# Optimization experiments

Hardware: AMD Instinct MI355X
Metric: run time of the kernel (lower is better)

## Reference

```python
import jax, jax.numpy as jnp
import numpy as np

NH, NL, NPNT = 8, 4, 4          # heads, levels, points
NQ, BS, NK, D, DFFN = 100, 8, 18, 256, 1024
SPATIAL = np.array([[92, 92], [46, 46], [23, 23], [12, 12]], np.int32)
LEN_MEM = int((SPATIAL[:, 0] * SPATIAL[:, 1]).sum())  # 11253


def _layernorm(x, g, b):
    m = x.mean(-1, keepdims=True)
    v = ((x - m) ** 2).mean(-1, keepdims=True)
    return (x - m) / jnp.sqrt(v + 1e-5) * g + b


def _mha(xq, xk, xv, in_w, in_b, out_w, out_b):
    # torch nn.MultiheadAttention semantics, inputs (S, B, D)
    S, B, d = xq.shape
    dh = d // NH
    wq, wk, wv = jnp.split(in_w, 3, axis=0)
    bq, bk, bv = jnp.split(in_b, 3, axis=0)
    def proj(x, w, b):
        return (x @ w.T + b).reshape(x.shape[0], B, NH, dh).transpose(1, 2, 0, 3)
    q = proj(xq, wq, bq) * (1.0 / np.sqrt(dh))
    k = proj(xk, wk, bk)
    v = proj(xv, wv, bv)
    att = jax.nn.softmax(jnp.einsum('bhqd,bhkd->bhqk', q, k), axis=-1)
    o = jnp.einsum('bhqk,bhkd->bhqd', att, v).transpose(2, 0, 1, 3).reshape(S, B, d)
    return o @ out_w.T + out_b


def _bilinear(v_l, loc):
    # v_l: (bs,H,W,NH,dh); loc: (bs,Lq,NH,P,2) normalized [0,1]
    # matches F.grid_sample(align_corners=False, padding_mode='zeros')
    bs, H, W, nh, dh = v_l.shape
    x = loc[..., 0] * W - 0.5
    y = loc[..., 1] * H - 0.5
    x0 = jnp.floor(x); y0 = jnp.floor(y)
    lx = x - x0; ly = y - y0
    b_idx = jnp.arange(bs)[:, None, None, None]
    h_idx = jnp.arange(nh)[None, None, :, None]
    def corner(xa, ya, w):
        valid = (xa >= 0) & (xa < W) & (ya >= 0) & (ya < H)
        xi = jnp.clip(xa, 0, W - 1).astype(jnp.int32)
        yi = jnp.clip(ya, 0, H - 1).astype(jnp.int32)
        return v_l[b_idx, yi, xi, h_idx] * (w * valid)[..., None]
    return (corner(x0, y0, (1 - lx) * (1 - ly)) + corner(x0 + 1, y0, lx * (1 - ly))
            + corner(x0, y0 + 1, (1 - lx) * ly) + corner(x0 + 1, y0 + 1, lx * ly))


def _msda(q, rp, mem, pad_mask, ss, off_w, off_b, aw_w, aw_b, val_w, val_b, outp_w, outp_b):
    bs, Lq, d = q.shape
    dh = d // NH
    value = mem @ val_w.T + val_b
    value = jnp.where(pad_mask[..., None], 0.0, value).reshape(bs, -1, NH, dh)
    off = (q @ off_w.T + off_b).reshape(bs, Lq, NH, NL, NPNT, 2)
    aw = jax.nn.softmax((q @ aw_w.T + aw_b).reshape(bs, Lq, NH, NL * NPNT), -1)
    aw = aw.reshape(bs, Lq, NH, NL, NPNT)
    wh = jnp.asarray(ss[:, ::-1].copy(), jnp.float32)  # offset normalizer (W, H)
    loc = rp[:, :, None, :, None, :] + off / wh[None, None, None, :, None, :]
    out = jnp.zeros((bs, Lq, NH, dh), q.dtype)
    start = 0
    for l in range(NL):
        H, W = int(ss[l, 0]), int(ss[l, 1])
        v_l = value[:, start:start + H * W].reshape(bs, H, W, NH, dh)
        start += H * W
        samp = _bilinear(v_l, loc[:, :, :, l])          # (bs,Lq,NH,P,dh)
        out = out + (samp * aw[:, :, :, l, :, None]).sum(3)
    return out.reshape(bs, Lq, d) @ outp_w.T + outp_b


def _forward(tgt_pose, pos, ref_points, memory, w_in_w, w_in_b, w_out_w, w_out_b,
             a_in_w, a_in_b, a_out_w, a_out_b, off_w, off_b, aw_w, aw_b,
             val_w, val_b, outp_w, outp_b, wn_g, wn_b, an_g, an_b,
             n1_g, n1_b, n2_g, n2_b, l1_w, l1_b, l2_w, l2_b,
             spatial_shapes, level_start_index, padding_mask):
    ss = np.asarray(jax.device_get(spatial_shapes))
    nq, bs, nk, d = tgt_pose.shape
    # within-group self-attn over the nk keypoint tokens.
    # NOTE: with_pos_embed mutates tgt_pose in place in the torch code, so
    # q = k = v = tgt + pos and the residual also uses tgt + pos (faithful).
    t = tgt_pose + pos
    x = t.reshape(nq * bs, nk, d).transpose(1, 0, 2)   # (nk, nq*bs, d)
    a1 = _mha(x, x, x, w_in_w, w_in_b, w_out_w, w_out_b)
    t = _layernorm(t + a1.transpose(1, 0, 2).reshape(nq, bs, nk, d), wn_g, wn_b)
    # across-group self-attn over the nq groups
    x2 = t.reshape(nq, bs * nk, d)
    a2 = _mha(x2, x2, x2, a_in_w, a_in_b, a_out_w, a_out_b)
    t = _layernorm(t + a2.reshape(nq, bs, nk, d), an_g, an_b)
    # MSDeformAttn cross-attention (in-place pos add again, faithful)
    t = t + pos
    q = t.transpose(1, 0, 2, 3).reshape(bs, nq * nk, d)
    rp = jnp.swapaxes(ref_points, 0, 1)                # (bs, nq*nk, NL, 2)
    mem = jnp.swapaxes(memory, 0, 1)                   # (bs, LEN_MEM, d)
    c = _msda(q, rp, mem, padding_mask, ss, off_w, off_b, aw_w, aw_b,
              val_w, val_b, outp_w, outp_b)
    c = c.reshape(bs, nq, nk, d).transpose(1, 0, 2, 3)
    t = _layernorm(t + c, n1_g, n1_b)
    # FFN (dropout is identity in eval)
    h = jax.nn.relu(t @ l1_w.T + l1_b)
    return _layernorm(t + (h @ l2_w.T + l2_b), n2_g, n2_b)


def setup_inputs() -> dict:
    key = jax.random.key(0)
    ks = jax.random.split(key, 16)
    p = lambda k, shape: jax.random.normal(k, shape, jnp.float32) * 0.02
    lsi = np.concatenate([[0], np.cumsum(SPATIAL[:, 0] * SPATIAL[:, 1])[:-1]]).astype(np.int32)
    return {
        'tgt_pose': jax.random.normal(ks[0], (NQ, BS, NK, D), jnp.float32),
        'pos': jax.random.normal(ks[1], (NQ, BS, NK, D), jnp.float32),
        'ref_points': jax.random.uniform(ks[2], (NQ * NK, BS, NL, 2), jnp.float32),
        'memory': jax.random.normal(ks[3], (LEN_MEM, BS, D), jnp.float32),
        'w_in_w': p(ks[4], (3 * D, D)), 'w_in_b': jnp.zeros((3 * D,)),
        'w_out_w': p(ks[5], (D, D)), 'w_out_b': jnp.zeros((D,)),
        'a_in_w': p(ks[6], (3 * D, D)), 'a_in_b': jnp.zeros((3 * D,)),
        'a_out_w': p(ks[7], (D, D)), 'a_out_b': jnp.zeros((D,)),
        'off_w': p(ks[8], (NH * NL * NPNT * 2, D)),
        'off_b': jax.random.uniform(ks[9], (NH * NL * NPNT * 2,), jnp.float32, -2.0, 2.0),
        'aw_w': p(ks[10], (NH * NL * NPNT, D)), 'aw_b': jnp.zeros((NH * NL * NPNT,)),
        'val_w': p(ks[11], (D, D)), 'val_b': jnp.zeros((D,)),
        'outp_w': p(ks[12], (D, D)), 'outp_b': jnp.zeros((D,)),
        'wn_g': jnp.ones((D,)), 'wn_b': jnp.zeros((D,)),
        'an_g': jnp.ones((D,)), 'an_b': jnp.zeros((D,)),
        'n1_g': jnp.ones((D,)), 'n1_b': jnp.zeros((D,)),
        'n2_g': jnp.ones((D,)), 'n2_b': jnp.zeros((D,)),
        'l1_w': p(ks[13], (DFFN, D)), 'l1_b': jnp.zeros((DFFN,)),
        'l2_w': p(ks[14], (D, DFFN)), 'l2_b': jnp.zeros((D,)),
        'spatial_shapes': jnp.asarray(SPATIAL),
        'level_start_index': jnp.asarray(lsi),
        'padding_mask': jnp.zeros((BS, LEN_MEM), bool),
    }


def reference(tgt_pose, pos, ref_points, memory, w_in_w, w_in_b, w_out_w, w_out_b,
              a_in_w, a_in_b, a_out_w, a_out_b, off_w, off_b, aw_w, aw_b,
              val_w, val_b, outp_w, outp_b, wn_g, wn_b, an_g, an_b,
              n1_g, n1_b, n2_g, n2_b, l1_w, l1_b, l2_w, l2_b,
              spatial_shapes, level_start_index, padding_mask):
    return _forward(tgt_pose, pos, ref_points, memory, w_in_w, w_in_b, w_out_w, w_out_b,
                    a_in_w, a_in_b, a_out_w, a_out_b, off_w, off_b, aw_w, aw_b,
                    val_w, val_b, outp_w, outp_b, wn_g, wn_b, an_g, an_b,
                    n1_g, n1_b, n2_g, n2_b, l1_w, l1_b, l2_w, l2_b,
                    spatial_shapes, level_start_index, padding_mask)
```

## Files before the change

kernel.cpp:

```cpp
#include <hip/hip_runtime.h>
#include <math.h>

#define NH_ 8
#define D_ 256
#define NK_ 18
#define NQ_ 100
#define BS_ 8
#define LQ_ 1800
#define LEN_MEM_ 11253
#define NTOK_ 14400

typedef short bf16x8 __attribute__((ext_vector_type(8)));
typedef float f32x4 __attribute__((ext_vector_type(4)));
typedef unsigned short ushort;

__device__ inline ushort f2bf(float f) {
    unsigned int u = __builtin_bit_cast(unsigned int, f);
    unsigned int r = (u + 0x7fffu + ((u >> 16) & 1u)) >> 16;
    return (ushort)r;
}
__device__ inline float bf2f(unsigned int u16) {
    unsigned int i = u16 << 16;
    return __builtin_bit_cast(float, i);
}

__global__ __launch_bounds__(256)
void wcvt_kernel(const float* s0, const float* s1, const float* s2, const float* s3,
                 const float* s4, const float* s5, const float* s6, const float* s7,
                 const float* s8, const float* s9, ushort* dst) {
    const int sizes[10] = {196608,65536,196608,65536,65536,32768,65536,65536,262144,262144};
    const int offs[10]  = {0,196608,262144,458752,524288,589824,622592,688128,753664,1015808};
    int ti = blockIdx.y;
    const float* s;
    switch (ti) {
        case 0: s = s0; break; case 1: s = s1; break; case 2: s = s2; break;
        case 3: s = s3; break; case 4: s = s4; break; case 5: s = s5; break;
        case 6: s = s6; break; case 7: s = s7; break; case 8: s = s8; break;
        default: s = s9; break;
    }
    int n = sizes[ti];
    int i = (blockIdx.x * 256 + threadIdx.x) * 8;
    if (i >= n) return;
    ushort* d = dst + offs[ti] + i;
    float4 f0 = *(const float4*)(s + i);
    float4 f1 = *(const float4*)(s + i + 4);
    int4 val;
    val.x = (int)f2bf(f0.x) | ((int)f2bf(f0.y) << 16);
    val.y = (int)f2bf(f0.z) | ((int)f2bf(f0.w) << 16);
    val.z = (int)f2bf(f1.x) | ((int)f2bf(f1.y) << 16);
    val.w = (int)f2bf(f1.z) | ((int)f2bf(f1.w) << 16);
    *(int4*)d = val;
}

__global__ __launch_bounds__(256)
void addcvt_kernel(const float* __restrict__ a, const float* __restrict__ b,
                   float* __restrict__ c, ushort* __restrict__ cbf, int n4) {
    int i = blockIdx.x * blockDim.x + threadIdx.x;
    if (i >= n4) return;
    float4 av = ((const float4*)a)[i];
    float4 bv = ((const float4*)b)[i];
    float4 cv;
    cv.x = av.x + bv.x; cv.y = av.y + bv.y; cv.z = av.z + bv.z; cv.w = av.w + bv.w;
    ((float4*)c)[i] = cv;
    uint2 p;
    p.x = (unsigned int)f2bf(cv.x) | ((unsigned int)f2bf(cv.y) << 16);
    p.y = (unsigned int)f2bf(cv.z) | ((unsigned int)f2bf(cv.w) << 16);
    *(uint2*)(cbf + (size_t)i * 4) = p;
}

template<int MODE, bool RELU, bool A_F32, bool OUT_BF16>
__global__ __launch_bounds__(256)
void gemm_kernel(const void* __restrict__ Av, const ushort* __restrict__ W,
                 const float* __restrict__ bias, void* __restrict__ Cv,
                 int M, int N, int K, const unsigned char* __restrict__ mask) {
    __shared__ ushort As[128 * 40];
    __shared__ ushort Bs[128 * 40];
    const int m0 = blockIdx.x * 128, n0 = blockIdx.y * 128;
    const int tid = threadIdx.x;
    const int w = tid >> 6, lane = tid & 63;
    const int wr = w >> 1, wc = w & 1;
    const int fr = lane & 15, hi = lane >> 4;
    f32x4 acc[4][4];
#pragma unroll
    for (int i = 0; i < 4; ++i)
#pragma unroll
        for (int j = 0; j < 4; ++j) acc[i][j] = f32x4{0.f, 0.f, 0.f, 0.f};

    for (int k0 = 0; k0 < K; k0 += 32) {
#pragma unroll
        for (int cc = 0; cc < 2; ++cc) {
            int c = tid + cc * 256;
            int row = c >> 2, kq = c & 3;
            int gr = m0 + row;
            int4 val = make_int4(0, 0, 0, 0);
            if (gr < M) {
                long arow;
                if (MODE == 1) {
                    int b = gr / LEN_MEM_; int m = gr - b * LEN_MEM_;
                    arow = (long)m * BS_ + b;
                } else if (MODE == 2) {
                    int b = gr / LQ_; int lq = gr - b * LQ_;
                    int q = lq / NK_; int kk = lq - q * NK_;
                    arow = (long)q * (BS_ * NK_) + b * NK_ + kk;
                } else {
                    arow = gr;
                }
                if (A_F32) {
                    const float* ap = (const float*)Av + arow * (long)K + k0 + kq * 8;
                    float4 f0 = *(const float4*)ap;
                    float4 f1 = *(const float4*)(ap + 4);
                    val.x = (int)f2bf(f0.x) | ((int)f2bf(f0.y) << 16);
                    val.y = (int)f2bf(f0.z) | ((int)f2bf(f0.w) << 16);
                    val.z = (int)f2bf(f1.x) | ((int)f2bf(f1.y) << 16);
                    val.w = (int)f2bf(f1.z) | ((int)f2bf(f1.w) << 16);
                } else {
                    val = *(const int4*)((const ushort*)Av + arow * (long)K + k0 + kq * 8);
                }
            }
            *(int4*)(As + row * 40 + kq * 8) = val;
        }
#pragma unroll
        for (int cc = 0; cc < 2; ++cc) {
            int c = tid + cc * 256;
            int row = c >> 2, kq = c & 3;
            *(int4*)(Bs + row * 40 + kq * 8) =
                *(const int4*)(W + (long)(n0 + row) * K + k0 + kq * 8);
        }
        __syncthreads();
        bf16x8 af[4], bfr[4];
#pragma unroll
        for (int i = 0; i < 4; ++i)
            af[i] = *(const bf16x8*)(As + (wr * 64 + i * 16 + fr) * 40 + hi * 8);
#pragma unroll
        for (int j = 0; j < 4; ++j)
            bfr[j] = *(const bf16x8*)(Bs + (wc * 64 + j * 16 + fr) * 40 + hi * 8);
#pragma unroll
        for (int i = 0; i < 4; ++i)
#pragma unroll
            for (int j = 0; j < 4; ++j)
                acc[i][j] = __builtin_amdgcn_mfma_f32_16x16x32_bf16(af[i], bfr[j], acc[i][j], 0, 0, 0);
        __syncthreads();
    }

#pragma unroll
    for (int i = 0; i < 4; ++i) {
#pragma unroll
        for (int r = 0; r < 4; ++r) {
            int gm = m0 + wr * 64 + i * 16 + hi * 4 + r;
            if (gm >= M) continue;
            long orow = gm;
            bool zero = false;
            if (MODE == 1) {
                if (mask && mask[gm]) zero = true;
            } else if (MODE == 3) {
                int b = gm / LQ_; int lq = gm - b * LQ_;
                int q = lq / NK_; int kk = lq - q * NK_;
                orow = (long)q * (BS_ * NK_) + b * NK_ + kk;
            }
#pragma unroll
            for (int j = 0; j < 4; ++j) {
                int gn = n0 + wc * 64 + j * 16 + fr;
                float v = acc[i][j][r] + bias[gn];
                if (RELU) v = fmaxf(v, 0.f);
                if (zero) v = 0.f;
                if (OUT_BF16) ((ushort*)Cv)[orow * (long)N + gn] = f2bf(v);
                else ((float*)Cv)[orow * (long)N + gn] = v;
            }
        }
    }
}

template<int S, int SP, int HPB>
__global__ __launch_bounds__(256)
void mattn_kernel(const ushort* __restrict__ qkv, ushort* __restrict__ outb,
                  int rsG, int rsS) {
    constexpr int SPk = ((SP + 31) / 32) * 32;
    constexpr int KST = 40;
    constexpr int PST = SPk + 8;
    constexpr int NT = SP / 16;
    constexpr int NB = HPB * NT;
    constexpr int HB = 8 / HPB;
    __shared__ ushort KsA[HPB * SP * KST];
    __shared__ ushort VtA[HPB * 32 * PST];
    __shared__ ushort PA [HPB * SP * PST];

    const int tid = threadIdx.x;
    const int g = blockIdx.x / HB;
    const int hbase = (blockIdx.x % HB) * HPB;

    for (int idx = tid; idx < HPB * S * 4; idx += 256) {
        int hh = idx / (S * 4); int rem = idx - hh * (S * 4);
        int j = rem >> 2, q = rem & 3;
        const ushort* base = qkv + ((size_t)g * rsG + (size_t)j * rsS) * 768 + (hbase + hh) * 32 + q * 8;
        uint4 kv = *(const uint4*)(base + 256);
        ushort* kd = KsA + hh * (SP * KST) + j * KST + q * 8;
        *(uint2*)kd = make_uint2(kv.x, kv.y);
        *(uint2*)(kd + 4) = make_uint2(kv.z, kv.w);
        uint4 vv = *(const uint4*)(base + 512);
        ushort* vt = VtA + hh * (32 * PST) + j;
        unsigned int uu[4] = {vv.x, vv.y, vv.z, vv.w};
#pragma unroll
        for (int e = 0; e < 4; ++e) {
            vt[(q * 8 + e * 2    ) * PST] = (ushort)(uu[e] & 0xffff);
            vt[(q * 8 + e * 2 + 1) * PST] = (ushort)(uu[e] >> 16);
        }
    }
    for (int idx = tid; idx < HPB * 32 * (SPk - S); idx += 256) {
        int hh = idx / (32 * (SPk - S)); int rem = idx - hh * (32 * (SPk - S));
        int d = rem / (SPk - S); int c = S + rem - d * (SPk - S);
        VtA[hh * 32 * PST + d * PST + c] = 0;
    }
    if constexpr (SPk > SP) {
        constexpr int PW = SPk - SP;
        for (int idx = tid; idx < HPB * SP * PW; idx += 256) {
            int hh = idx / (SP * PW); int rem = idx - hh * (SP * PW);
            int rrow = rem / PW; int c = SP + rem - rrow * PW;
            PA[hh * SP * PST + rrow * PST + c] = 0;
        }
    }
    __syncthreads();

    const int wv = tid >> 6, lane = tid & 63, fr = lane & 15, hi = lane >> 4;
    for (int band = wv; band < NB; band += 4) {
        const int hh = band / NT, mb = band - (band / NT) * NT;
        const int h = hbase + hh;
        const ushort* Ks = KsA + hh * (SP * KST);
        const ushort* Vt = VtA + hh * (32 * PST);
        ushort* P = PA + hh * (SP * PST);

        int sq = mb * 16 + fr; if (sq > S - 1) sq = S - 1;
        bf16x8 qf = *(const bf16x8*)(qkv + ((size_t)g * rsG + (size_t)sq * rsS) * 768 + h * 32 + hi * 8);
        f32x4 sc[NT];
#pragma unroll
        for (int t = 0; t < NT; ++t) {
            bf16x8 kf = *(const bf16x8*)(Ks + (t * 16 + fr) * KST + hi * 8);
            sc[t] = __builtin_amdgcn_mfma_f32_16x16x32_bf16(qf, kf, f32x4{0.f, 0.f, 0.f, 0.f}, 0, 0, 0);
        }
#pragma unroll
        for (int t = 0; t < NT; ++t) {
            bool valid = (t * 16 + fr) < S;
#pragma unroll
            for (int r = 0; r < 4; ++r)
                sc[t][r] = valid ? sc[t][r] * 0.17677669529663687f : -1e30f;
        }
#pragma unroll
        for (int r = 0; r < 4; ++r) {
            float m = sc[0][r];
#pragma unroll
            for (int t = 1; t < NT; ++t) m = fmaxf(m, sc[t][r]);
            m = fmaxf(m, __shfl_xor(m, 1)); m = fmaxf(m, __shfl_xor(m, 2));
            m = fmaxf(m, __shfl_xor(m, 4)); m = fmaxf(m, __shfl_xor(m, 8));
            float e[NT]; float sum = 0.f;
#pragma unroll
            for (int t = 0; t < NT; ++t) { e[t] = __expf(sc[t][r] - m); sum += e[t]; }
            sum += __shfl_xor(sum, 1); sum += __shfl_xor(sum, 2);
            sum += __shfl_xor(sum, 4); sum += __shfl_xor(sum, 8);
            float inv = 1.f / sum;
            int row = mb * 16 + hi * 4 + r;
#pragma unroll
            for (int t = 0; t < NT; ++t)
                P[row * PST + t * 16 + fr] = f2bf(e[t] * inv);
        }
        f32x4 o0 = {0.f, 0.f, 0.f, 0.f}, o1 = {0.f, 0.f, 0.f, 0.f};
#pragma unroll
        for (int kb = 0; kb < SPk / 32; ++kb) {
            bf16x8 pf = *(const bf16x8*)(P + (mb * 16 + fr) * PST + kb * 32 + hi * 8);
            bf16x8 v0 = *(const bf16x8*)(Vt + fr * PST + kb * 32 + hi * 8);
            bf16x8 v1 = *(const bf16x8*)(Vt + (16 + fr) * PST + kb * 32 + hi * 8);
            o0 = __builtin_amdgcn_mfma_f32_16x16x32_bf16(pf, v0, o0, 0, 0, 0);
            o1 = __builtin_amdgcn_mfma_f32_16x16x32_bf16(pf, v1, o1, 0, 0, 0);
        }
#pragma unroll
        for (int r = 0; r < 4; ++r) {
            int s = mb * 16 + hi * 4 + r;
            if (s < S) {
                size_t ob = ((size_t)g * rsG + (size_t)s * rsS) * 256 + h * 32;
                outb[ob + fr] = f2bf(o0[r]);
                outb[ob + 16 + fr] = f2bf(o1[r]);
            }
        }
    }
}

__global__ __launch_bounds__(256)
void addln_kernel(const float* __restrict__ base, const float* __restrict__ delta,
                  const float* __restrict__ gamma, const float* __restrict__ beta,
                  float* __restrict__ out, ushort* __restrict__ obf, int M) {
    int row = blockIdx.x * 4 + (threadIdx.x >> 6);
    int lane = threadIdx.x & 63;
    if (row >= M) return;
    const float* pb = base + (size_t)row * 256;
    const float* pd = delta + (size_t)row * 256;
    float v[4]; float s = 0.f;
#pragma unroll
    for (int i = 0; i < 4; ++i) { int c = lane + i * 64; v[i] = pb[c] + pd[c]; s += v[i]; }
#pragma unroll
    for (int off = 32; off; off >>= 1) s += __shfl_xor(s, off);
    float mean = s * (1.f / 256.f);
    float var = 0.f;
#pragma unroll
    for (int i = 0; i < 4; ++i) { float d = v[i] - mean; var += d * d; }
#pragma unroll
    for (int off = 32; off; off >>= 1) var += __shfl_xor(var, off);
    var *= (1.f / 256.f);
    float rstd = rsqrtf(var + 1e-5f);
#pragma unroll
    for (int i = 0; i < 4; ++i) {
        int c = lane + i * 64;
        float o = (v[i] - mean) * rstd * gamma[c] + beta[c];
        out[(size_t)row * 256 + c] = o;
        if (obf) obf[(size_t)row * 256 + c] = f2bf(o);
    }
}

__global__ __launch_bounds__(256)
void awsm_kernel(const float* __restrict__ aw, float* __restrict__ awn) {
    int u = blockIdx.x * 256 + threadIdx.x;
    if (u >= NTOK_ * 8) return;
    int row = u >> 3, h = u & 7;
    const float* p = aw + (size_t)row * 128 + h * 16;
    float w[16], m = -1e30f;
#pragma unroll
    for (int i = 0; i < 16; ++i) { w[i] = p[i]; m = fmaxf(m, w[i]); }
    float sum = 0.f;
#pragma unroll
    for (int i = 0; i < 16; ++i) { w[i] = __expf(w[i] - m); sum += w[i]; }
    float inv = 1.f / sum;
    float* o = awn + (size_t)u * 16;
#pragma unroll
    for (int i = 0; i < 16; ++i) o[i] = w[i] * inv;
}

__global__ __launch_bounds__(256)
void msda_kernel(const float* __restrict__ offb, const float* __restrict__ awn,
                 const ushort* __restrict__ val, const float* __restrict__ refp,
                 const int* __restrict__ spatial, const int* __restrict__ lsi,
                 ushort* __restrict__ samp) {
    int unit = blockIdx.x * 16 + (threadIdx.x >> 4);
    int lane = threadIdx.x & 15;
    int h = unit & 7;
    int t = unit >> 3;
    int lq = t % LQ_;
    int b = t / LQ_;
    const float* offp = offb + ((size_t)b * LQ_ + lq) * 256 + h * 32;
    const float* wp = awn + (size_t)unit * 16;
    float acc0 = 0.f, acc1 = 0.f;
#pragma unroll
    for (int lvl = 0; lvl < 4; ++lvl) {
        int H = spatial[lvl * 2], W = spatial[lvl * 2 + 1];
        int st = lsi[lvl];
        float rpx = refp[(((size_t)lq * BS_ + b) * 4 + lvl) * 2 + 0];
        float rpy = refp[(((size_t)lq * BS_ + b) * 4 + lvl) * 2 + 1];
        const ushort* vb = val + ((size_t)b * LEN_MEM_ + st) * 256 + h * 32 + lane * 2;
        float fW = (float)W, fH = (float)H;
#pragma unroll
        for (int p = 0; p < 4; ++p) {
            float ox = offp[(lvl * 4 + p) * 2 + 0];
            float oy = offp[(lvl * 4 + p) * 2 + 1];
            float x = rpx * fW + ox - 0.5f;
            float y = rpy * fH + oy - 0.5f;
            float x0f = floorf(x), y0f = floorf(y);
            float lx = x - x0f, ly = y - y0f;
            int x0 = (int)x0f, y0 = (int)y0f;
            int xc0 = min(max(x0, 0), W - 1), xc1 = min(max(x0 + 1, 0), W - 1);
            int yc0 = min(max(y0, 0), H - 1), yc1 = min(max(y0 + 1, 0), H - 1);
            float vx0 = (x0 >= 0 && x0 < W) ? 1.f : 0.f;
            float vx1 = (x0 >= -1 && x0 + 1 < W) ? 1.f : 0.f;
            float vy0 = (y0 >= 0 && y0 < H) ? 1.f : 0.f;
            float vy1 = (y0 >= -1 && y0 + 1 < H) ? 1.f : 0.f;
            float wpt = wp[lvl * 4 + p];
            float w00 = wpt * (1.f - lx) * (1.f - ly) * vx0 * vy0;
            float w10 = wpt * lx * (1.f - ly) * vx1 * vy0;
            float w01 = wpt * (1.f - lx) * ly * vx0 * vy1;
            float w11 = wpt * lx * ly * vx1 * vy1;
            unsigned int u00 = *(const unsigned int*)(vb + ((size_t)yc0 * W + xc0) * 256);
            unsigned int u10 = *(const unsigned int*)(vb + ((size_t)yc0 * W + xc1) * 256);
            unsigned int u01 = *(const unsigned int*)(vb + ((size_t)yc1 * W + xc0) * 256);
            unsigned int u11 = *(const unsigned int*)(vb + ((size_t)yc1 * W + xc1) * 256);
            acc0 += w00 * bf2f(u00 & 0xffff) + w10 * bf2f(u10 & 0xffff)
                  + w01 * bf2f(u01 & 0xffff) + w11 * bf2f(u11 & 0xffff);
            acc1 += w00 * bf2f(u00 >> 16) + w10 * bf2f(u10 >> 16)
                  + w01 * bf2f(u01 >> 16) + w11 * bf2f(u11 >> 16);
        }
    }
    size_t o = ((size_t)b * LQ_ + lq) * 256 + h * 32 + lane * 2;
    unsigned int pack = (unsigned int)f2bf(acc0) | ((unsigned int)f2bf(acc1) << 16);
    *(unsigned int*)(samp + o) = pack;
}

extern "C" void kernel_launch(void* const* d_in, const int* in_sizes, int n_in,
                              void* d_out, int out_size, void* d_ws, size_t ws_size,
                              hipStream_t stream) {
    const float* tgt     = (const float*)d_in[0];
    const float* pos     = (const float*)d_in[1];
    const float* refp    = (const float*)d_in[2];
    const float* memory  = (const float*)d_in[3];
    const float* w_in_w  = (const float*)d_in[4];
    const float* w_in_b  = (const float*)d_in[5];
    const float* w_out_w = (const float*)d_in[6];
    const float* w_out_b = (const float*)d_in[7];
    const float* a_in_w  = (const float*)d_in[8];
    const float* a_in_b  = (const float*)d_in[9];
    const float* a_out_w = (const float*)d_in[10];
    const float* a_out_b = (const float*)d_in[11];
    const float* off_w   = (const float*)d_in[12];
    const float* off_b   = (const float*)d_in[13];
    const float* aw_w    = (const float*)d_in[14];
    const float* aw_b    = (const float*)d_in[15];
    const float* val_w   = (const float*)d_in[16];
    const float* val_b   = (const float*)d_in[17];
    const float* outp_w  = (const float*)d_in[18];
    const float* outp_b  = (const float*)d_in[19];
    const float* wn_g    = (const float*)d_in[20];
    const float* wn_b    = (const float*)d_in[21];
    const float* an_g    = (const float*)d_in[22];
    const float* an_b    = (const float*)d_in[23];
    const float* n1_g    = (const float*)d_in[24];
    const float* n1_b    = (const float*)d_in[25];
    const float* n2_g    = (const float*)d_in[26];
    const float* n2_b    = (const float*)d_in[27];
    const float* l1_w    = (const float*)d_in[28];
    const float* l1_b    = (const float*)d_in[29];
    const float* l2_w    = (const float*)d_in[30];
    const float* l2_b    = (const float*)d_in[31];
    const int*   spatial = (const int*)d_in[32];
    const int*   lsi     = (const int*)d_in[33];
    const unsigned char* pmask = (const unsigned char*)d_in[34];
    float* out = (float*)d_out;

    float*  T      = (float*)d_ws;
    ushort* Tbf    = (ushort*)(T + 3686400);
    ushort* B16    = Tbf + 3686400;
    ushort* CBbf   = B16 + 11059200;
    ushort* VALbf  = CBbf + 3686400;
    ushort* SAMPbf = VALbf + 23046144;
    ushort* Hbf    = SAMPbf + 3686400;
    ushort* WB     = Hbf + 14745600;
    float*  OFF    = (float*)(WB + 1277952);
    float*  AW     = OFF + 3686400;
    float*  AWn    = AW + 1843200;

    ushort* WB_win  = WB + 0;
    ushort* WB_wout = WB + 196608;
    ushort* WB_ain  = WB + 262144;
    ushort* WB_aout = WB + 458752;
    ushort* WB_off  = WB + 524288;
    ushort* WB_aw   = WB + 589824;
    ushort* WB_val  = WB + 622592;
    ushort* WB_outp = WB + 688128;
    ushort* WB_l1   = WB + 753664;
    ushort* WB_l2   = WB + 1015808;

    const int n4 = NTOK_ * 256 / 4;

    wcvt_kernel<<<dim3(128, 10), 256, 0, stream>>>(
        w_in_w, w_out_w, a_in_w, a_out_w, off_w, aw_w, val_w, outp_w, l1_w, l2_w, WB);
    addcvt_kernel<<<n4 / 256, 256, 0, stream>>>(tgt, pos, T, Tbf, n4);
    gemm_kernel<0, false, false, true><<<dim3(113, 6), 256, 0, stream>>>(
        Tbf, WB_win, w_in_b, B16, NTOK_, 768, 256, nullptr);
    mattn_kernel<18, 32, 4><<<800 * 2, 256, 0, stream>>>(B16, CBbf, 18, 1);
    gemm_kernel<0, false, false, false><<<dim3(113, 2), 256, 0, stream>>>(
        CBbf, WB_wout, w_out_b, OFF, NTOK_, 256, 256, nullptr);
    addln_kernel<<<NTOK_ / 4, 256, 0, stream>>>(T, OFF, wn_g, wn_b, T, Tbf, NTOK_);
    gemm_kernel<0, false, false, true><<<dim3(113, 6), 256, 0, stream>>>(
        Tbf, WB_ain, a_in_b, B16, NTOK_, 768, 256, nullptr);
    mattn_kernel<100, 112, 1><<<144 * 8, 256, 0, stream>>>(B16, CBbf, 1, 144);
    gemm_kernel<0, false, false, false><<<dim3(113, 2), 256, 0, stream>>>(
        CBbf, WB_aout, a_out_b, OFF, NTOK_, 256, 256, nullptr);
    addln_kernel<<<NTOK_ / 4, 256, 0, stream>>>(T, OFF, an_g, an_b, T, Tbf, NTOK_);
    addcvt_kernel<<<n4 / 256, 256, 0, stream>>>(T, pos, T, Tbf, n4);
    gemm_kernel<1, false, true, true><<<dim3(704, 2), 256, 0, stream>>>(
        memory, WB_val, val_b, VALbf, 90024, 256, 256, pmask);
    gemm_kernel<2, false, false, false><<<dim3(113, 2), 256, 0, stream>>>(
        Tbf, WB_off, off_b, OFF, NTOK_, 256, 256, nullptr);
    gemm_kernel<2, false, false, false><<<dim3(113, 1), 256, 0, stream>>>(
        Tbf, WB_aw, aw_b, AW, NTOK_, 128, 256, nullptr);
    awsm_kernel<<<(NTOK_ * 8 + 255) / 256, 256, 0, stream>>>(AW, AWn);
    msda_kernel<<<NTOK_ * 8 / 16, 256, 0, stream>>>(OFF, AWn, VALbf, refp, spatial, lsi, SAMPbf);
    gemm_kernel<3, false, false, false><<<dim3(113, 2), 256, 0, stream>>>(
        SAMPbf, WB_outp, outp_b, OFF, NTOK_, 256, 256, nullptr);
    addln_kernel<<<NTOK_ / 4, 256, 0, stream>>>(T, OFF, n1_g, n1_b, T, Tbf, NTOK_);
    gemm_kernel<0, true, false, true><<<dim3(113, 8), 256, 0, stream>>>(
        Tbf, WB_l1, l1_b, Hbf, NTOK_, 1024, 256, nullptr);
    gemm_kernel<0, false, false, false><<<dim3(113, 2), 256, 0, stream>>>(
        Hbf, WB_l2, l2_b, OFF, NTOK_, 256, 1024, nullptr);
    addln_kernel<<<NTOK_ / 4, 256, 0, stream>>>(T, OFF, n2_g, n2_b, out, nullptr, NTOK_);
}
```

Measured before the change: 370.8 us.

## Fuse softmax into MSDA, keep value in memory layout, widen GEMM K tile

The attention-weight softmax kernel is removed: the softmax is now computed inside the MSDA kernel with wave shuffles, and offsets are loaded once per lane and broadcast with shuffles. The value projection now runs on the memory tensor in its native (position, batch) row order, and MSDA and the mask lookup index that layout, which removes the per-row divide remap in the value GEMM. The GEMM now stages a 64-wide K tile with padded LDS rows and one row per thread pair, halving the number of barriers per K. The separate pos-add/convert pass is folded into the preceding add+layernorm. The trade-off is a more strided value gather in MSDA and higher LDS use per GEMM block.

```diff
diff --git a/kernel.cpp b/kernel.cpp
--- a/kernel.cpp
+++ b/kernel.cpp
@@ -22,6 +22,9 @@
 __device__ inline float bf2f(unsigned int u16) {
     unsigned int i = u16 << 16;
     return __builtin_bit_cast(float, i);
+}
+__device__ inline int packbf2(float a, float b) {
+    return (int)f2bf(a) | ((int)f2bf(b) << 16);
 }
 
 __global__ __launch_bounds__(256)
@@ -45,10 +48,10 @@
     float4 f0 = *(const float4*)(s + i);
     float4 f1 = *(const float4*)(s + i + 4);
     int4 val;
-    val.x = (int)f2bf(f0.x) | ((int)f2bf(f0.y) << 16);
-    val.y = (int)f2bf(f0.z) | ((int)f2bf(f0.w) << 16);
-    val.z = (int)f2bf(f1.x) | ((int)f2bf(f1.y) << 16);
-    val.w = (int)f2bf(f1.z) | ((int)f2bf(f1.w) << 16);
+    val.x = packbf2(f0.x, f0.y);
+    val.y = packbf2(f0.z, f0.w);
+    val.z = packbf2(f1.x, f1.y);
+    val.w = packbf2(f1.z, f1.w);
     *(int4*)d = val;
 }
 
@@ -63,8 +66,8 @@
     cv.x = av.x + bv.x; cv.y = av.y + bv.y; cv.z = av.z + bv.z; cv.w = av.w + bv.w;
     ((float4*)c)[i] = cv;
     uint2 p;
-    p.x = (unsigned int)f2bf(cv.x) | ((unsigned int)f2bf(cv.y) << 16);
-    p.y = (unsigned int)f2bf(cv.z) | ((unsigned int)f2bf(cv.w) << 16);
+    p.x = (unsigned int)packbf2(cv.x, cv.y);
+    p.y = (unsigned int)packbf2(cv.z, cv.w);
     *(uint2*)(cbf + (size_t)i * 4) = p;
 }
 
@@ -73,8 +76,9 @@
 void gemm_kernel(const void* __restrict__ Av, const ushort* __restrict__ W,
                  const float* __restrict__ bias, void* __restrict__ Cv,
                  int M, int N, int K, const unsigned char* __restrict__ mask) {
-    __shared__ ushort As[128 * 40];
-    __shared__ ushort Bs[128 * 40];
+    constexpr int AST = 72;
+    __shared__ ushort As[128 * AST];
+    __shared__ ushort Bs[128 * AST];
     const int m0 = blockIdx.x * 128, n0 = blockIdx.y * 128;
     const int tid = threadIdx.x;
     const int w = tid >> 6, lane = tid & 63;
@@ -86,59 +90,67 @@
 #pragma unroll
         for (int j = 0; j < 4; ++j) acc[i][j] = f32x4{0.f, 0.f, 0.f, 0.f};
 
-    for (int k0 = 0; k0 < K; k0 += 32) {
-#pragma unroll
-        for (int cc = 0; cc < 2; ++cc) {
-            int c = tid + cc * 256;
-            int row = c >> 2, kq = c & 3;
-            int gr = m0 + row;
-            int4 val = make_int4(0, 0, 0, 0);
-            if (gr < M) {
-                long arow;
-                if (MODE == 1) {
-                    int b = gr / LEN_MEM_; int m = gr - b * LEN_MEM_;
-                    arow = (long)m * BS_ + b;
-                } else if (MODE == 2) {
-                    int b = gr / LQ_; int lq = gr - b * LQ_;
-                    int q = lq / NK_; int kk = lq - q * NK_;
-                    arow = (long)q * (BS_ * NK_) + b * NK_ + kk;
-                } else {
-                    arow = gr;
+    const int srow = tid >> 1, shalf = tid & 1;
+    long arow = 0;
+    const bool avalid = (m0 + srow) < M;
+    {
+        int gr = m0 + srow;
+        if (gr >= M) gr = M - 1;
+        if (MODE == 2) {
+            int b = gr / LQ_; int lq = gr - b * LQ_;
+            int q = lq / NK_; int kk = lq - q * NK_;
+            arow = (long)q * (BS_ * NK_) + b * NK_ + kk;
+        } else {
+            arow = gr;
+        }
+    }
+
+    for (int k0 = 0; k0 < K; k0 += 64) {
+        ushort* ad = As + srow * AST + shalf * 32;
+        if (avalid) {
+            if (A_F32) {
+                const float* ap = (const float*)Av + arow * (long)K + k0 + shalf * 32;
+#pragma unroll
+                for (int i = 0; i < 4; ++i) {
+                    float4 f0 = *(const float4*)(ap + i * 8);
+                    float4 f1 = *(const float4*)(ap + i * 8 + 4);
+                    int4 v;
+                    v.x = packbf2(f0.x, f0.y); v.y = packbf2(f0.z, f0.w);
+                    v.z = packbf2(f1.x, f1.y); v.w = packbf2(f1.z, f1.w);
+                    *(int4*)(ad + i * 8) = v;
                 }
-                if (A_F32) {
-                    const float* ap = (const float*)Av + arow * (long)K + k0 + kq * 8;
-                    float4 f0 = *(const float4*)ap;
-                    float4 f1 = *(const float4*)(ap + 4);
-                    val.x = (int)f2bf(f0.x) | ((int)f2bf(f0.y) << 16);
-                    val.y = (int)f2bf(f0.z) | ((int)f2bf(f0.w) << 16);
-                    val.z = (int)f2bf(f1.x) | ((int)f2bf(f1.y) << 16);
-                    val.w = (int)f2bf(f1.z) | ((int)f2bf(f1.w) << 16);
-                } else {
-                    val = *(const int4*)((const ushort*)Av + arow * (long)K + k0 + kq * 8);
-                }
+            } else {
+                const ushort* ap = (const ushort*)Av + arow * (long)K + k0 + shalf * 32;
+#pragma unroll
+                for (int i = 0; i < 4; ++i) *(int4*)(ad + i * 8) = *(const int4*)(ap + i * 8);
             }
-            *(int4*)(As + row * 40 + kq * 8) = val;
-        }
-#pragma unroll
-        for (int cc = 0; cc < 2; ++cc) {
-            int c = tid + cc * 256;
-            int row = c >> 2, kq = c & 3;
-            *(int4*)(Bs + row * 40 + kq * 8) =
-                *(const int4*)(W + (long)(n0 + row) * K + k0 + kq * 8);
+        } else {
+            int4 z = make_int4(0, 0, 0, 0);
+#pragma unroll
+            for (int i = 0; i < 4; ++i) *(int4*)(ad + i * 8) = z;
+        }
+        {
+            const ushort* wp = W + (long)(n0 + srow) * K + k0 + shalf * 32;
+            ushort* bd = Bs + srow * AST + shalf * 32;
+#pragma unroll
+            for (int i = 0; i < 4; ++i) *(int4*)(bd + i * 8) = *(const int4*)(wp + i * 8);
         }
         __syncthreads();
-        bf16x8 af[4], bfr[4];
-#pragma unroll
-        for (int i = 0; i < 4; ++i)
-            af[i] = *(const bf16x8*)(As + (wr * 64 + i * 16 + fr) * 40 + hi * 8);
-#pragma unroll
-        for (int j = 0; j < 4; ++j)
-            bfr[j] = *(const bf16x8*)(Bs + (wc * 64 + j * 16 + fr) * 40 + hi * 8);
-#pragma unroll
-        for (int i = 0; i < 4; ++i)
+#pragma unroll
+        for (int kb = 0; kb < 2; ++kb) {
+            bf16x8 af[4], bfr[4];
+#pragma unroll
+            for (int i = 0; i < 4; ++i)
+                af[i] = *(const bf16x8*)(As + (wr * 64 + i * 16 + fr) * AST + kb * 32 + hi * 8);
 #pragma unroll
             for (int j = 0; j < 4; ++j)
-                acc[i][j] = __builtin_amdgcn_mfma_f32_16x16x32_bf16(af[i], bfr[j], acc[i][j], 0, 0, 0);
+                bfr[j] = *(const bf16x8*)(Bs + (wc * 64 + j * 16 + fr) * AST + kb * 32 + hi * 8);
+#pragma unroll
+            for (int i = 0; i < 4; ++i)
+#pragma unroll
+                for (int j = 0; j < 4; ++j)
+                    acc[i][j] = __builtin_amdgcn_mfma_f32_16x16x32_bf16(af[i], bfr[j], acc[i][j], 0, 0, 0);
+        }
         __syncthreads();
     }
 
@@ -151,7 +163,7 @@
             long orow = gm;
             bool zero = false;
             if (MODE == 1) {
-                if (mask && mask[gm]) zero = true;
+                if (mask && mask[(size_t)(gm & 7) * LEN_MEM_ + (gm >> 3)]) zero = true;
             } else if (MODE == 3) {
                 int b = gm / LQ_; int lq = gm - b * LQ_;
                 int q = lq / NK_; int kk = lq - q * NK_;
@@ -285,6 +297,7 @@
 __global__ __launch_bounds__(256)
 void addln_kernel(const float* __restrict__ base, const float* __restrict__ delta,
                   const float* __restrict__ gamma, const float* __restrict__ beta,
+                  const float* __restrict__ pos,
                   float* __restrict__ out, ushort* __restrict__ obf, int M) {
     int row = blockIdx.x * 4 + (threadIdx.x >> 6);
     int lane = threadIdx.x & 63;
@@ -308,42 +321,38 @@
     for (int i = 0; i < 4; ++i) {
         int c = lane + i * 64;
         float o = (v[i] - mean) * rstd * gamma[c] + beta[c];
+        if (pos) o += pos[(size_t)row * 256 + c];
         out[(size_t)row * 256 + c] = o;
         if (obf) obf[(size_t)row * 256 + c] = f2bf(o);
     }
 }
 
 __global__ __launch_bounds__(256)
-void awsm_kernel(const float* __restrict__ aw, float* __restrict__ awn) {
-    int u = blockIdx.x * 256 + threadIdx.x;
-    if (u >= NTOK_ * 8) return;
-    int row = u >> 3, h = u & 7;
-    const float* p = aw + (size_t)row * 128 + h * 16;
-    float w[16], m = -1e30f;
-#pragma unroll
-    for (int i = 0; i < 16; ++i) { w[i] = p[i]; m = fmaxf(m, w[i]); }
-    float sum = 0.f;
-#pragma unroll
-    for (int i = 0; i < 16; ++i) { w[i] = __expf(w[i] - m); sum += w[i]; }
-    float inv = 1.f / sum;
-    float* o = awn + (size_t)u * 16;
-#pragma unroll
-    for (int i = 0; i < 16; ++i) o[i] = w[i] * inv;
-}
-
-__global__ __launch_bounds__(256)
-void msda_kernel(const float* __restrict__ offb, const float* __restrict__ awn,
+void msda_kernel(const float* __restrict__ offb, const float* __restrict__ aw,
                  const ushort* __restrict__ val, const float* __restrict__ refp,
                  const int* __restrict__ spatial, const int* __restrict__ lsi,
                  ushort* __restrict__ samp) {
     int unit = blockIdx.x * 16 + (threadIdx.x >> 4);
     int lane = threadIdx.x & 15;
+    int lbase = (threadIdx.x & 63) & 48;
     int h = unit & 7;
     int t = unit >> 3;
     int lq = t % LQ_;
     int b = t / LQ_;
+
+    float logit = aw[((size_t)b * LQ_ + lq) * 128 + h * 16 + lane];
+    float m = logit;
+    m = fmaxf(m, __shfl_xor(m, 1)); m = fmaxf(m, __shfl_xor(m, 2));
+    m = fmaxf(m, __shfl_xor(m, 4)); m = fmaxf(m, __shfl_xor(m, 8));
+    float e = __expf(logit - m);
+    float sum = e;
+    sum += __shfl_xor(sum, 1); sum += __shfl_xor(sum, 2);
+    sum += __shfl_xor(sum, 4); sum += __shfl_xor(sum, 8);
+    float wnorm = e / sum;
+
     const float* offp = offb + ((size_t)b * LQ_ + lq) * 256 + h * 32;
-    const float* wp = awn + (size_t)unit * 16;
+    float2 myoff = ((const float2*)offp)[lane];
+
     float acc0 = 0.f, acc1 = 0.f;
 #pragma unroll
     for (int lvl = 0; lvl < 4; ++lvl) {
@@ -351,12 +360,14 @@
         int st = lsi[lvl];
         float rpx = refp[(((size_t)lq * BS_ + b) * 4 + lvl) * 2 + 0];
         float rpy = refp[(((size_t)lq * BS_ + b) * 4 + lvl) * 2 + 1];
-        const ushort* vb = val + ((size_t)b * LEN_MEM_ + st) * 256 + h * 32 + lane * 2;
+        const ushort* vb = val + ((size_t)st * 8 + b) * 256 + h * 32 + lane * 2;
         float fW = (float)W, fH = (float)H;
 #pragma unroll
         for (int p = 0; p < 4; ++p) {
-            float ox = offp[(lvl * 4 + p) * 2 + 0];
-            float oy = offp[(lvl * 4 + p) * 2 + 1];
+            int pi = lvl * 4 + p;
+            float ox = __shfl(myoff.x, lbase + pi);
+            float oy = __shfl(myoff.y, lbase + pi);
+            float wpt = __shfl(wnorm, lbase + pi);
             float x = rpx * fW + ox - 0.5f;
             float y = rpy * fH + oy - 0.5f;
             float x0f = floorf(x), y0f = floorf(y);
@@ -368,15 +379,14 @@
             float vx1 = (x0 >= -1 && x0 + 1 < W) ? 1.f : 0.f;
             float vy0 = (y0 >= 0 && y0 < H) ? 1.f : 0.f;
             float vy1 = (y0 >= -1 && y0 + 1 < H) ? 1.f : 0.f;
-            float wpt = wp[lvl * 4 + p];
             float w00 = wpt * (1.f - lx) * (1.f - ly) * vx0 * vy0;
             float w10 = wpt * lx * (1.f - ly) * vx1 * vy0;
             float w01 = wpt * (1.f - lx) * ly * vx0 * vy1;
             float w11 = wpt * lx * ly * vx1 * vy1;
-            unsigned int u00 = *(const unsigned int*)(vb + ((size_t)yc0 * W + xc0) * 256);
-            unsigned int u10 = *(const unsigned int*)(vb + ((size_t)yc0 * W + xc1) * 256);
-            unsigned int u01 = *(const unsigned int*)(vb + ((size_t)yc1 * W + xc0) * 256);
-            unsigned int u11 = *(const unsigned int*)(vb + ((size_t)yc1 * W + xc1) * 256);
+            unsigned int u00 = *(const unsigned int*)(vb + ((size_t)(yc0 * W + xc0) * 8) * 256);
+            unsigned int u10 = *(const unsigned int*)(vb + ((size_t)(yc0 * W + xc1) * 8) * 256);
+            unsigned int u01 = *(const unsigned int*)(vb + ((size_t)(yc1 * W + xc0) * 8) * 256);
+            unsigned int u11 = *(const unsigned int*)(vb + ((size_t)(yc1 * W + xc1) * 8) * 256);
             acc0 += w00 * bf2f(u00 & 0xffff) + w10 * bf2f(u10 & 0xffff)
                   + w01 * bf2f(u01 & 0xffff) + w11 * bf2f(u11 & 0xffff);
             acc1 += w00 * bf2f(u00 >> 16) + w10 * bf2f(u10 >> 16)
@@ -384,8 +394,7 @@
         }
     }
     size_t o = ((size_t)b * LQ_ + lq) * 256 + h * 32 + lane * 2;
-    unsigned int pack = (unsigned int)f2bf(acc0) | ((unsigned int)f2bf(acc1) << 16);
-    *(unsigned int*)(samp + o) = pack;
+    *(unsigned int*)(samp + o) = (unsigned int)packbf2(acc0, acc1);
 }
 
 extern "C" void kernel_launch(void* const* d_in, const int* in_sizes, int n_in,
@@ -438,7 +447,6 @@
     ushort* WB     = Hbf + 14745600;
     float*  OFF    = (float*)(WB + 1277952);
     float*  AW     = OFF + 3686400;
-    float*  AWn    = AW + 1843200;
 
     ushort* WB_win  = WB + 0;
     ushort* WB_wout = WB + 196608;
@@ -461,28 +469,26 @@
     mattn_kernel<18, 32, 4><<<800 * 2, 256, 0, stream>>>(B16, CBbf, 18, 1);
     gemm_kernel<0, false, false, false><<<dim3(113, 2), 256, 0, stream>>>(
         CBbf, WB_wout, w_out_b, OFF, NTOK_, 256, 256, nullptr);
-    addln_kernel<<<NTOK_ / 4, 256, 0, stream>>>(T, OFF, wn_g, wn_b, T, Tbf, NTOK_);
+    addln_kernel<<<NTOK_ / 4, 256, 0, stream>>>(T, OFF, wn_g, wn_b, nullptr, T, Tbf, NTOK_);
     gemm_kernel<0, false, false, true><<<dim3(113, 6), 256, 0, stream>>>(
         Tbf, WB_ain, a_in_b, B16, NTOK_, 768, 256, nullptr);
     mattn_kernel<100, 112, 1><<<144 * 8, 256, 0, stream>>>(B16, CBbf, 1, 144);
     gemm_kernel<0, false, false, false><<<dim3(113, 2), 256, 0, stream>>>(
         CBbf, WB_aout, a_out_b, OFF, NTOK_, 256, 256, nullptr);
-    addln_kernel<<<NTOK_ / 4, 256, 0, stream>>>(T, OFF, an_g, an_b, T, Tbf, NTOK_);
-    addcvt_kernel<<<n4 / 256, 256, 0, stream>>>(T, pos, T, Tbf, n4);
+    addln_kernel<<<NTOK_ / 4, 256, 0, stream>>>(T, OFF, an_g, an_b, pos, T, Tbf, NTOK_);
     gemm_kernel<1, false, true, true><<<dim3(704, 2), 256, 0, stream>>>(
         memory, WB_val, val_b, VALbf, 90024, 256, 256, pmask);
     gemm_kernel<2, false, false, false><<<dim3(113, 2), 256, 0, stream>>>(
         Tbf, WB_off, off_b, OFF, NTOK_, 256, 256, nullptr);
     gemm_kernel<2, false, false, false><<<dim3(113, 1), 256, 0, stream>>>(
         Tbf, WB_aw, aw_b, AW, NTOK_, 128, 256, nullptr);
-    awsm_kernel<<<(NTOK_ * 8 + 255) / 256, 256, 0, stream>>>(AW, AWn);
-    msda_kernel<<<NTOK_ * 8 / 16, 256, 0, stream>>>(OFF, AWn, VALbf, refp, spatial, lsi, SAMPbf);
+    msda_kernel<<<NTOK_ * 8 / 16, 256, 0, stream>>>(OFF, AW, VALbf, refp, spatial, lsi, SAMPbf);
     gemm_kernel<3, false, false, false><<<dim3(113, 2), 256, 0, stream>>>(
         SAMPbf, WB_outp, outp_b, OFF, NTOK_, 256, 256, nullptr);
-    addln_kernel<<<NTOK_ / 4, 256, 0, stream>>>(T, OFF, n1_g, n1_b, T, Tbf, NTOK_);
+    addln_kernel<<<NTOK_ / 4, 256, 0, stream>>>(T, OFF, n1_g, n1_b, nullptr, T, Tbf, NTOK_);
     gemm_kernel<0, true, false, true><<<dim3(113, 8), 256, 0, stream>>>(
         Tbf, WB_l1, l1_b, Hbf, NTOK_, 1024, 256, nullptr);
     gemm_kernel<0, false, false, false><<<dim3(113, 2), 256, 0, stream>>>(
         Hbf, WB_l2, l2_b, OFF, NTOK_, 256, 1024, nullptr);
-    addln_kernel<<<NTOK_ / 4, 256, 0, stream>>>(T, OFF, n2_g, n2_b, out, nullptr, NTOK_);
-}
+    addln_kernel<<<NTOK_ / 4, 256, 0, stream>>>(T, OFF, n2_g, n2_b, nullptr, out, nullptr, NTOK_);
+}
```

Result: faster. 361.1 us (-2.6%).
